# Optimization experiments

Measured on AMD Instinct MI355X. Metric: run time of the kernel, lower is better.

The kernel has to match this reference:

```python
import jax, jax.numpy as jnp
import numpy as np

D_MODEL = 2048
NUM_EXPERTS = 64
TOP_K = 2


def setup_inputs() -> dict:
    key = jax.random.key(0)
    kx, kw, kb = jax.random.split(key, 3)
    x = jax.random.normal(kx, (4, 4096, D_MODEL), dtype=jnp.float32)
    # nn.Linear(d_model, num_experts): weight [num_experts, d_model], bias [num_experts]
    bound = 1.0 / np.sqrt(D_MODEL)
    W = jax.random.uniform(kw, (NUM_EXPERTS, D_MODEL), minval=-bound, maxval=bound, dtype=jnp.float32)
    b = jax.random.uniform(kb, (NUM_EXPERTS,), minval=-bound, maxval=bound, dtype=jnp.float32)
    return {"x": x, "W": W, "b": b}


def reference(x, W, b):
    # Eval mode: no noise injection (self.training is False).
    logits = jnp.einsum('bsd,ed->bse', x, W) + b          # [B, S, E]
    raw_weights = jax.nn.softmax(logits, axis=-1)          # [B, S, E]
    top_k_weights, top_k_indices = jax.lax.top_k(raw_weights, TOP_K)  # [B, S, K]
    normalized = top_k_weights / jnp.sum(top_k_weights, axis=-1, keepdims=True)
    return normalized, top_k_indices
```

## Files before the change

### kernel.cpp

```cpp
#include <hip/hip_runtime.h>
#include <math.h>

#define DM 2048
#define NEXP 64
#define NTOK 16384
#define NSLICE 4
#define KSL (DM / NSLICE)
#define KC 32
#define NCH (KSL / KC)
#define TPW 32
#define MBT 128
#define NBLK1 ((NTOK / MBT) * NSLICE)
#define NKG (DM / KC)
#define WFRAG_BYTES (NKG * 12 * 1024)
#define PART_BYTES (NSLICE * NEXP * NTOK * 4)

typedef __attribute__((ext_vector_type(8))) short short8;
typedef __attribute__((ext_vector_type(4))) float f32x4;

__device__ __forceinline__ void async16(void* lds, const void* g) {
  __builtin_amdgcn_global_load_lds(
      (const __attribute__((address_space(1))) unsigned int*)g,
      (__attribute__((address_space(3))) unsigned int*)lds, 16, 0, 0);
}

__device__ __forceinline__ void split3t(float f, unsigned short& h,
                                        unsigned short& m, unsigned short& l) {
  unsigned u = __float_as_uint(f);
  h = (unsigned short)(u >> 16);
  float f1 = f - __uint_as_float(u & 0xFFFF0000u);
  unsigned u1 = __float_as_uint(f1);
  m = (unsigned short)(u1 >> 16);
  float f2 = f1 - __uint_as_float(u1 & 0xFFFF0000u);
  l = (unsigned short)(__float_as_uint(f2) >> 16);
}

__device__ __forceinline__ void split8(const f32x4& a0, const f32x4& a1,
                                       short8& h, short8& m, short8& l) {
  float v[8] = {a0[0], a0[1], a0[2], a0[3], a1[0], a1[1], a1[2], a1[3]};
#pragma unroll
  for (int j = 0; j < 8; ++j) {
    unsigned short hh, mm, ll;
    split3t(v[j], hh, mm, ll);
    h[j] = (short)hh; m[j] = (short)mm; l[j] = (short)ll;
  }
}

__global__ void convw_kernel(const float* __restrict__ W,
                             unsigned short* __restrict__ wfrag) {
  const int kg = blockIdx.x;
  const int lane = threadIdx.x & 63;
  const int nt = threadIdx.x >> 6;
  const int e = nt * 16 + (lane & 15);
  const int kpos = kg * 32 + (lane >> 4) * 8;
  const f32x4* wp = (const f32x4*)(W + (size_t)e * DM + kpos);
  f32x4 w0 = wp[0], w1 = wp[1];
  short8 h, m, l;
  split8(w0, w1, h, m, l);
  size_t base = ((size_t)(kg * 12 + nt) * 64 + lane) * 8;
  *(short8*)(wfrag + base) = h;
  *(short8*)(wfrag + base + (size_t)4 * 64 * 8) = m;
  *(short8*)(wfrag + base + (size_t)8 * 64 * 8) = l;
}

__global__ __launch_bounds__(256, 2)
void router_gemm(const float* __restrict__ x,
                 const unsigned short* __restrict__ wfrag,
                 float* __restrict__ part) {
  const int lane = threadIdx.x & 63;
  const int wv = threadIdx.x >> 6;
  const int col = lane & 15;
  const int quad = lane >> 4;
  const int tg = blockIdx.x >> 2;
  const int s = blockIdx.x & 3;
  const int tok0 = tg * MBT + wv * TPW;

  __shared__ __align__(16) float xs[4][2][TPW][KC];

  const int rowoff = lane >> 3;
  const int unit = (lane & 7) ^ (rowoff & 7);
  const float* xsrc = x + (size_t)(tok0 + rowoff) * DM + s * KSL + unit * 4;

  auto stage = [&](int buf, int c) {
#pragma unroll
    for (int i = 0; i < 4; ++i)
      async16(&xs[wv][buf][i * 8][0], xsrc + (size_t)(i * 8) * DM + c * KC);
  };

  f32x4 acc[2][4];
#pragma unroll
  for (int mt = 0; mt < 2; ++mt)
#pragma unroll
    for (int nt = 0; nt < 4; ++nt) acc[mt][nt] = (f32x4){0.f, 0.f, 0.f, 0.f};

  const unsigned short* bbase = wfrag + (size_t)(s * NCH) * 12 * 512 +
                                (size_t)lane * 8;

  stage(0, 0);

  for (int c = 0; c < NCH; ++c) {
    const int cur = c & 1;

    short8 B[3][4];
#pragma unroll
    for (int limb = 0; limb < 3; ++limb)
#pragma unroll
      for (int nt = 0; nt < 4; ++nt)
        B[limb][nt] = *(const short8*)(bbase +
            ((size_t)c * 12 + limb * 4 + nt) * 512);

    asm volatile("" ::: "memory");

    if (c + 1 < NCH) {
      stage(cur ^ 1, c + 1);
      asm volatile("s_waitcnt vmcnt(16)" ::: "memory");
    } else {
      asm volatile("s_waitcnt vmcnt(12)" ::: "memory");
    }

#pragma unroll
    for (int mt = 0; mt < 2; ++mt) {
      const int row = mt * 16 + col;
      const int u0 = (quad * 2) ^ (col & 7);
      const int u1 = (quad * 2 + 1) ^ (col & 7);
      f32x4 a0 = *(const f32x4*)&xs[wv][cur][row][u0 * 4];
      f32x4 a1 = *(const f32x4*)&xs[wv][cur][row][u1 * 4];
      short8 ah, am, al;
      split8(a0, a1, ah, am, al);
#pragma unroll
      for (int nt = 0; nt < 4; ++nt) {
        f32x4 cc = acc[mt][nt];
        cc = __builtin_amdgcn_mfma_f32_16x16x32_bf16(ah, B[0][nt], cc, 0, 0, 0);
        cc = __builtin_amdgcn_mfma_f32_16x16x32_bf16(ah, B[1][nt], cc, 0, 0, 0);
        cc = __builtin_amdgcn_mfma_f32_16x16x32_bf16(am, B[0][nt], cc, 0, 0, 0);
        cc = __builtin_amdgcn_mfma_f32_16x16x32_bf16(ah, B[2][nt], cc, 0, 0, 0);
        cc = __builtin_amdgcn_mfma_f32_16x16x32_bf16(al, B[0][nt], cc, 0, 0, 0);
        cc = __builtin_amdgcn_mfma_f32_16x16x32_bf16(am, B[1][nt], cc, 0, 0, 0);
        acc[mt][nt] = cc;
      }
    }
  }

#pragma unroll
  for (int mt = 0; mt < 2; ++mt)
#pragma unroll
    for (int nt = 0; nt < 4; ++nt) {
      const size_t e = (size_t)(s * NEXP + nt * 16 + col);
      *(f32x4*)(part + e * NTOK + tok0 + mt * 16 + quad * 4) = acc[mt][nt];
    }
}

__global__ __launch_bounds__(256, 4)
void router_reduce(const float* __restrict__ part,
                   const float* __restrict__ bias, float* __restrict__ out) {
  const int lane = threadIdx.x & 63;
  const int wv = threadIdx.x >> 6;
  const int q = lane >> 4;
  const int t = blockIdx.x * 64 + wv * 16 + (lane & 15);

  float v1 = -INFINITY, v2 = -INFINITY;
  int i1 = 0, i2 = 0;
#pragma unroll
  for (int e = 0; e < NEXP; ++e) {
    float p = part[(size_t)(q * NEXP + e) * NTOK + t];
    p += __shfl_xor(p, 16, 64);
    p += __shfl_xor(p, 32, 64);
    const float v = p + bias[e];
    const bool a = v > v1;
    const bool b = v > v2;
    const float nv2 = a ? v1 : (b ? v : v2);
    const int ni2 = a ? i1 : (b ? e : i2);
    v2 = nv2; i2 = ni2;
    i1 = a ? e : i1;
    v1 = a ? v : v1;
  }
  if (q == 0) {
    const float ex = expf(v2 - v1);
    const float den = 1.f + ex;
    *(float2*)(out + 2 * t) = make_float2(1.f / den, ex / den);
    *(float2*)(out + 2 * NTOK + 2 * t) = make_float2((float)i1, (float)i2);
  }
}

__global__ __launch_bounds__(512, 2)
void router_fb(const float* __restrict__ x, const float* __restrict__ W,
               const float* __restrict__ bias, float* __restrict__ out) {
  const int lane = threadIdx.x & 63;
  const int wv = threadIdx.x >> 6;
  const int col = lane & 15;
  const int quad = lane >> 4;
  const int tok0 = blockIdx.x * 32;
  const int k0 = wv * 256;

  __shared__ float part[8][32][68];

  f32x4 acc[2][4];
#pragma unroll
  for (int ms = 0; ms < 2; ++ms)
#pragma unroll
    for (int nt = 0; nt < 4; ++nt) acc[ms][nt] = (f32x4){0.f, 0.f, 0.f, 0.f};

  for (int ks = 0; ks < 8; ++ks) {
    const int k = k0 + ks * 32 + quad * 8;
    short8 ah[2], am2[2], al2[2];
#pragma unroll
    for (int ms = 0; ms < 2; ++ms) {
      const f32x4* ap = (const f32x4*)(x + (size_t)(tok0 + ms * 16 + col) * DM + k);
      f32x4 a0 = ap[0], a1 = ap[1];
      split8(a0, a1, ah[ms], am2[ms], al2[ms]);
    }
#pragma unroll
    for (int nt = 0; nt < 4; ++nt) {
      short8 bh, bm, bl;
      const f32x4* wp = (const f32x4*)(W + (size_t)(nt * 16 + col) * DM + k);
      f32x4 w0 = wp[0], w1 = wp[1];
      split8(w0, w1, bh, bm, bl);
#pragma unroll
      for (int ms = 0; ms < 2; ++ms) {
        f32x4 cc = acc[ms][nt];
        cc = __builtin_amdgcn_mfma_f32_16x16x32_bf16(ah[ms], bh, cc, 0, 0, 0);
        cc = __builtin_amdgcn_mfma_f32_16x16x32_bf16(ah[ms], bm, cc, 0, 0, 0);
        cc = __builtin_amdgcn_mfma_f32_16x16x32_bf16(am2[ms], bh, cc, 0, 0, 0);
        cc = __builtin_amdgcn_mfma_f32_16x16x32_bf16(ah[ms], bl, cc, 0, 0, 0);
        cc = __builtin_amdgcn_mfma_f32_16x16x32_bf16(al2[ms], bh, cc, 0, 0, 0);
        cc = __builtin_amdgcn_mfma_f32_16x16x32_bf16(am2[ms], bm, cc, 0, 0, 0);
        acc[ms][nt] = cc;
      }
    }
  }
#pragma unroll
  for (int ms = 0; ms < 2; ++ms)
#pragma unroll
    for (int nt = 0; nt < 4; ++nt)
#pragma unroll
      for (int r = 0; r < 4; ++r)
        part[wv][ms * 16 + quad * 4 + r][nt * 16 + col] = acc[ms][nt][r];
  __syncthreads();
  const float bl_ = bias[lane];
#pragma unroll
  for (int ti = 0; ti < 4; ++ti) {
    const int t = wv * 4 + ti;
    float v1 = bl_;
#pragma unroll
    for (int p = 0; p < 8; ++p) v1 += part[p][t][lane];
    int i1 = lane;
    float v2 = -INFINITY;
    int i2 = NEXP;
#pragma unroll
    for (int off = 32; off > 0; off >>= 1) {
      float ov1 = __shfl_xor(v1, off, 64);
      int   oi1 = __shfl_xor(i1, off, 64);
      float ov2 = __shfl_xor(v2, off, 64);
      int   oi2 = __shfl_xor(i2, off, 64);
      bool afirst = (v1 > ov1) || (v1 == ov1 && i1 < oi1);
      float w1v = afirst ? v1 : ov1;  int w1i = afirst ? i1 : oi1;
      float c1v = afirst ? v2 : ov2;  int c1i = afirst ? i2 : oi2;
      float c2v = afirst ? ov1 : v1;  int c2i = afirst ? oi1 : i1;
      bool sfirst = (c1v > c2v) || (c1v == c2v && c1i < c2i);
      v1 = w1v; i1 = w1i;
      v2 = sfirst ? c1v : c2v;
      i2 = sfirst ? c1i : c2i;
    }
    if (lane == 0) {
      const float ex = expf(v2 - v1);
      const float den = 1.f + ex;
      const int token = tok0 + t;
      *(float2*)(out + 2 * token) = make_float2(1.f / den, ex / den);
      *(float2*)(out + 2 * NTOK + 2 * token) =
          make_float2((float)i1, (float)i2);
    }
  }
}

extern "C" void kernel_launch(void* const* d_in, const int* in_sizes, int n_in,
                              void* d_out, int out_size, void* d_ws, size_t ws_size,
                              hipStream_t stream) {
  const float* x = (const float*)d_in[0];
  const float* W = (const float*)d_in[1];
  const float* b = (const float*)d_in[2];
  float* out = (float*)d_out;

  const size_t need = (size_t)WFRAG_BYTES + (size_t)PART_BYTES;
  if (ws_size >= need) {
    unsigned short* wfrag = (unsigned short*)d_ws;
    float* part = (float*)((char*)d_ws + WFRAG_BYTES);
    hipLaunchKernelGGL(convw_kernel, dim3(NKG), dim3(256), 0, stream, W, wfrag);
    hipLaunchKernelGGL(router_gemm, dim3(NBLK1), dim3(256), 0, stream,
                       x, wfrag, part);
    hipLaunchKernelGGL(router_reduce, dim3(NTOK / 64), dim3(256), 0, stream,
                       part, b, out);
  } else {
    hipLaunchKernelGGL(router_fb, dim3(NTOK / 32), dim3(512), 0, stream,
                       x, W, b, out);
  }
}
```

Baseline: 210.1 us.

## Share split activation limbs across waves via LDS, one expert tile per wave

Each block now handles 64 tokens, and each wave owns one 16-expert column tile instead of 32 tokens across all 64 experts. Activations are split into bf16 hi/mid/lo limbs once, written to a shared LDS buffer, and reused by all four waves, so the per-wave B-fragment loads and register footprint shrink. Occupancy is raised to 4 blocks per CU. In exchange the kernel adds two block-wide barriers per K chunk and extra LDS traffic for the limb staging.

```diff
diff --git a/kernel.cpp b/kernel.cpp
--- a/kernel.cpp
+++ b/kernel.cpp
@@ -8,14 +8,14 @@
 #define KSL (DM / NSLICE)
 #define KC 32
 #define NCH (KSL / KC)
-#define TPW 32
-#define MBT 128
-#define NBLK1 ((NTOK / MBT) * NSLICE)
+#define MBLK 64
+#define NBLK1 ((NTOK / MBLK) * NSLICE)
 #define NKG (DM / KC)
 #define WFRAG_BYTES (NKG * 12 * 1024)
 #define PART_BYTES (NSLICE * NEXP * NTOK * 4)
 
 typedef __attribute__((ext_vector_type(8))) short short8;
+typedef __attribute__((ext_vector_type(4))) short short4v;
 typedef __attribute__((ext_vector_type(4))) float f32x4;
 
 __device__ __forceinline__ void async16(void* lds, const void* g) {
@@ -63,7 +63,7 @@
   *(short8*)(wfrag + base + (size_t)8 * 64 * 8) = l;
 }
 
-__global__ __launch_bounds__(256, 2)
+__global__ __launch_bounds__(256, 4)
 void router_gemm(const float* __restrict__ x,
                  const unsigned short* __restrict__ wfrag,
                  float* __restrict__ part) {
@@ -73,81 +73,85 @@
   const int quad = lane >> 4;
   const int tg = blockIdx.x >> 2;
   const int s = blockIdx.x & 3;
-  const int tok0 = tg * MBT + wv * TPW;
-
-  __shared__ __align__(16) float xs[4][2][TPW][KC];
-
-  const int rowoff = lane >> 3;
-  const int unit = (lane & 7) ^ (rowoff & 7);
-  const float* xsrc = x + (size_t)(tok0 + rowoff) * DM + s * KSL + unit * 4;
+  const int tok0 = tg * MBLK;
+
+  __shared__ __align__(16) float xs[2][MBLK][KC];
+  __shared__ __align__(16) unsigned short alim[3][4][64][8];
+
+  const float* xsrc =
+      x + (size_t)(tok0 + wv * 16 + (lane >> 3)) * DM + s * KSL + (lane & 7) * 4;
 
   auto stage = [&](int buf, int c) {
 #pragma unroll
-    for (int i = 0; i < 4; ++i)
-      async16(&xs[wv][buf][i * 8][0], xsrc + (size_t)(i * 8) * DM + c * KC);
+    for (int i = 0; i < 2; ++i)
+      async16(&xs[buf][wv * 16 + i * 8][0], xsrc + (size_t)(i * 8) * DM + c * KC);
   };
 
-  f32x4 acc[2][4];
-#pragma unroll
-  for (int mt = 0; mt < 2; ++mt)
-#pragma unroll
-    for (int nt = 0; nt < 4; ++nt) acc[mt][nt] = (f32x4){0.f, 0.f, 0.f, 0.f};
-
-  const unsigned short* bbase = wfrag + (size_t)(s * NCH) * 12 * 512 +
-                                (size_t)lane * 8;
+  f32x4 acc[4];
+#pragma unroll
+  for (int mt = 0; mt < 4; ++mt) acc[mt] = (f32x4){0.f, 0.f, 0.f, 0.f};
+
+  const unsigned short* bb = wfrag + (size_t)lane * 8;
 
   stage(0, 0);
 
   for (int c = 0; c < NCH; ++c) {
     const int cur = c & 1;
-
-    short8 B[3][4];
-#pragma unroll
-    for (int limb = 0; limb < 3; ++limb)
-#pragma unroll
-      for (int nt = 0; nt < 4; ++nt)
-        B[limb][nt] = *(const short8*)(bbase +
-            ((size_t)c * 12 + limb * 4 + nt) * 512);
-
+    const int kg = s * NCH + c;
+
+    short8 B0 = *(const short8*)(bb + ((size_t)kg * 12 + 0 + wv) * 512);
+    short8 B1 = *(const short8*)(bb + ((size_t)kg * 12 + 4 + wv) * 512);
+    short8 B2 = *(const short8*)(bb + ((size_t)kg * 12 + 8 + wv) * 512);
     asm volatile("" ::: "memory");
 
     if (c + 1 < NCH) {
       stage(cur ^ 1, c + 1);
-      asm volatile("s_waitcnt vmcnt(16)" ::: "memory");
+      asm volatile("s_waitcnt vmcnt(5)\n\ts_barrier" ::: "memory");
     } else {
-      asm volatile("s_waitcnt vmcnt(12)" ::: "memory");
-    }
-
-#pragma unroll
-    for (int mt = 0; mt < 2; ++mt) {
-      const int row = mt * 16 + col;
-      const int u0 = (quad * 2) ^ (col & 7);
-      const int u1 = (quad * 2 + 1) ^ (col & 7);
-      f32x4 a0 = *(const f32x4*)&xs[wv][cur][row][u0 * 4];
-      f32x4 a1 = *(const f32x4*)&xs[wv][cur][row][u1 * 4];
-      short8 ah, am, al;
-      split8(a0, a1, ah, am, al);
-#pragma unroll
-      for (int nt = 0; nt < 4; ++nt) {
-        f32x4 cc = acc[mt][nt];
-        cc = __builtin_amdgcn_mfma_f32_16x16x32_bf16(ah, B[0][nt], cc, 0, 0, 0);
-        cc = __builtin_amdgcn_mfma_f32_16x16x32_bf16(ah, B[1][nt], cc, 0, 0, 0);
-        cc = __builtin_amdgcn_mfma_f32_16x16x32_bf16(am, B[0][nt], cc, 0, 0, 0);
-        cc = __builtin_amdgcn_mfma_f32_16x16x32_bf16(ah, B[2][nt], cc, 0, 0, 0);
-        cc = __builtin_amdgcn_mfma_f32_16x16x32_bf16(al, B[0][nt], cc, 0, 0, 0);
-        cc = __builtin_amdgcn_mfma_f32_16x16x32_bf16(am, B[1][nt], cc, 0, 0, 0);
-        acc[mt][nt] = cc;
+      asm volatile("s_waitcnt vmcnt(3)\n\ts_barrier" ::: "memory");
+    }
+
+#pragma unroll
+    for (int i = 0; i < 2; ++i) {
+      const int row = wv * 16 + i * 8 + (lane >> 3);
+      const int u = lane & 7;
+      f32x4 v = *(const f32x4*)&xs[cur][row][u * 4];
+      short4v h, m, l;
+#pragma unroll
+      for (int j = 0; j < 4; ++j) {
+        unsigned short hh, mm, ll;
+        split3t(v[j], hh, mm, ll);
+        h[j] = (short)hh; m[j] = (short)mm; l[j] = (short)ll;
       }
-    }
-  }
-
-#pragma unroll
-  for (int mt = 0; mt < 2; ++mt)
-#pragma unroll
-    for (int nt = 0; nt < 4; ++nt) {
-      const size_t e = (size_t)(s * NEXP + nt * 16 + col);
-      *(f32x4*)(part + e * NTOK + tok0 + mt * 16 + quad * 4) = acc[mt][nt];
-    }
+      const int slot = (i * 8 + (lane >> 3)) + 16 * (u >> 1);
+      const int half = (u & 1) * 4;
+      *(short4v*)&alim[0][wv][slot][half] = h;
+      *(short4v*)&alim[1][wv][slot][half] = m;
+      *(short4v*)&alim[2][wv][slot][half] = l;
+    }
+    asm volatile("s_waitcnt lgkmcnt(0)\n\ts_barrier" ::: "memory");
+
+#pragma unroll
+    for (int mt = 0; mt < 4; ++mt) {
+      short8 ah = *(const short8*)&alim[0][mt][lane][0];
+      short8 am = *(const short8*)&alim[1][mt][lane][0];
+      short8 al = *(const short8*)&alim[2][mt][lane][0];
+      f32x4 cc = acc[mt];
+      cc = __builtin_amdgcn_mfma_f32_16x16x32_bf16(ah, B0, cc, 0, 0, 0);
+      cc = __builtin_amdgcn_mfma_f32_16x16x32_bf16(ah, B1, cc, 0, 0, 0);
+      cc = __builtin_amdgcn_mfma_f32_16x16x32_bf16(am, B0, cc, 0, 0, 0);
+      cc = __builtin_amdgcn_mfma_f32_16x16x32_bf16(ah, B2, cc, 0, 0, 0);
+      cc = __builtin_amdgcn_mfma_f32_16x16x32_bf16(al, B0, cc, 0, 0, 0);
+      cc = __builtin_amdgcn_mfma_f32_16x16x32_bf16(am, B1, cc, 0, 0, 0);
+      acc[mt] = cc;
+    }
+  }
+
+#pragma unroll
+  for (int mt = 0; mt < 4; ++mt) {
+    const size_t e = (size_t)(s * NEXP + wv * 16 + col);
+    *(f32x4*)(part + e * NTOK + tok0 + mt * 16 + quad * 4) = acc[mt];
+  }
 }
 
 __global__ __launch_bounds__(256, 4)
```

Measured after the change: 206.9 us. About the same (-1.5%).
